# Kernel tuning notes

Hardware: AMD Instinct MI355X
Metric: run time of the kernel (lower is better)

## Reference

```python
import jax, jax.numpy as jnp
import numpy as np

B, S, H, V, L = 2, 1024, 2048, 32000, 8


def _ternary(w):
    """BitNet-1.58 style per-tensor ternary quantization with STE."""
    scale = jnp.mean(jnp.abs(w))
    wq = jnp.clip(jnp.round(w / (scale + 1e-8)), -1.0, 1.0) * scale
    # straight-through: forward value is wq, gradient flows to w
    return w + jax.lax.stop_gradient(wq - w)


def _layernorm(x, g, b, eps=1e-5):
    m = jnp.mean(x, axis=-1, keepdims=True)
    v = jnp.var(x, axis=-1, keepdims=True)
    return (x - m) / jnp.sqrt(v + eps) * g + b


def setup_inputs() -> dict:
    key = jax.random.key(0)
    ks = jax.random.split(key, 5)
    return {
        "input_ids": jax.random.randint(ks[0], (B, S), 0, V),
        "embed": jax.random.normal(ks[1], (V, H), jnp.float32) * 0.02,
        "layer_w": jax.random.normal(ks[2], (L, H, H), jnp.float32) * 0.02,
        "layer_b": jnp.zeros((L, H), jnp.float32),
        "ln_g": jnp.ones((L, H), jnp.float32),
        "ln_b": jnp.zeros((L, H), jnp.float32),
        "final_g": jnp.ones((H,), jnp.float32),
        "final_b": jnp.zeros((H,), jnp.float32),
        "head_w": jax.random.normal(ks[3], (V, H), jnp.float32) * 0.02,
    }


def reference(input_ids, embed, layer_w, layer_b, ln_g, ln_b, final_g, final_b, head_w):
    # embedding lookup: (B, S, H)
    h = embed[input_ids]

    def step(h, params):
        w, b, g, bb = params
        y = jnp.einsum("bsh,oh->bso", h, _ternary(w)) + b  # ternary linear
        h = _layernorm(y + h, g, bb)                        # residual + LN
        return h, None

    h, _ = jax.lax.scan(step, h, (layer_w, layer_b, ln_g, ln_b))
    h = _layernorm(h, final_g, final_b)
    logits = jnp.einsum("bsh,vh->bsv", h, _ternary(head_w))  # (B, S, V)
    return logits
```

## Files before the change

### kernel.cpp

```cpp
#include <hip/hip_runtime.h>


#define H 2048
#define MTOK 2048
#define VOC 32000
#define NL 8
#define BK 32

typedef __attribute__((ext_vector_type(8))) _Float16 f16x8;
typedef __attribute__((ext_vector_type(4))) float f32x4;

__device__ __forceinline__ unsigned short f2h(float f) {
  _Float16 h = (_Float16)f;
  union { _Float16 h; unsigned short u; } v; v.h = h;
  return v.u;
}

__global__ void abssum_kernel(const float* __restrict__ w, int n, float* __restrict__ out) {
  __shared__ float sbuf[4];
  int tid = blockIdx.x * blockDim.x + threadIdx.x;
  int stride = gridDim.x * blockDim.x * 4;
  float s = 0.f;
  for (int i = tid * 4; i < n; i += stride) {
    float4 v = *reinterpret_cast<const float4*>(w + i);
    s += fabsf(v.x) + fabsf(v.y) + fabsf(v.z) + fabsf(v.w);
  }
#pragma unroll
  for (int off = 32; off > 0; off >>= 1) s += __shfl_down(s, off);
  if ((threadIdx.x & 63) == 0) sbuf[threadIdx.x >> 6] = s;
  __syncthreads();
  if (threadIdx.x == 0) atomicAdd(out, sbuf[0] + sbuf[1] + sbuf[2] + sbuf[3]);
}

__global__ void quantize_kernel(const float* __restrict__ w, int n,
                                const float* __restrict__ sumptr, float cnt,
                                unsigned short* __restrict__ T) {
  float scale = *sumptr / cnt;
  float spe = scale + 1e-8f;
  int tid = blockIdx.x * blockDim.x + threadIdx.x;
  int stride = gridDim.x * blockDim.x * 4;
  for (int i = tid * 4; i < n; i += stride) {
    float4 v = *reinterpret_cast<const float4*>(w + i);
    ushort4 t;
    t.x = f2h(fminf(fmaxf(rintf(v.x / spe), -1.f), 1.f));
    t.y = f2h(fminf(fmaxf(rintf(v.y / spe), -1.f), 1.f));
    t.z = f2h(fminf(fmaxf(rintf(v.z / spe), -1.f), 1.f));
    t.w = f2h(fminf(fmaxf(rintf(v.w / spe), -1.f), 1.f));
    *reinterpret_cast<ushort4*>(T + i) = t;
  }
}

__global__ void gather_split_kernel(const int* __restrict__ ids, const float* __restrict__ embed,
                                    float* __restrict__ h, unsigned short* __restrict__ act) {
  int t = blockIdx.x;
  long src = (long)ids[t] * H;
  long dst = (long)t * H;
  for (int c = threadIdx.x * 4; c < H; c += blockDim.x * 4) {
    float4 v = *reinterpret_cast<const float4*>(embed + src + c);
    *reinterpret_cast<float4*>(h + dst + c) = v;
    ushort4 u;
    u.x = f2h(v.x); u.y = f2h(v.y); u.z = f2h(v.z); u.w = f2h(v.w);
    *reinterpret_cast<ushort4*>(act + dst + c) = u;
  }
}

__device__ __forceinline__ float block_sum(float v, float* sbuf) {
#pragma unroll
  for (int off = 32; off > 0; off >>= 1) v += __shfl_down(v, off);
  int lane = threadIdx.x & 63, w = threadIdx.x >> 6;
  if (lane == 0) sbuf[w] = v;
  __syncthreads();
  float r = sbuf[0] + sbuf[1] + sbuf[2] + sbuf[3];
  __syncthreads();
  return r;
}

__global__ void ln_kernel(const float* __restrict__ x_in, const float* __restrict__ resid,
                          const float* __restrict__ g, const float* __restrict__ b,
                          float* __restrict__ hout, unsigned short* __restrict__ act) {
  __shared__ float sbuf[4];
  int t = blockIdx.x;
  long base = (long)t * H;
  int c0 = threadIdx.x * 8;
  float x[8];
#pragma unroll
  for (int j = 0; j < 8; j += 4) {
    float4 v = *reinterpret_cast<const float4*>(x_in + base + c0 + j);
    x[j] = v.x; x[j + 1] = v.y; x[j + 2] = v.z; x[j + 3] = v.w;
  }
  if (resid != nullptr) {
#pragma unroll
    for (int j = 0; j < 8; j += 4) {
      float4 v = *reinterpret_cast<const float4*>(resid + base + c0 + j);
      x[j] += v.x; x[j + 1] += v.y; x[j + 2] += v.z; x[j + 3] += v.w;
    }
  }
  float s = 0.f;
#pragma unroll
  for (int j = 0; j < 8; ++j) s += x[j];
  s = block_sum(s, sbuf);
  float m = s * (1.f / H);
  float vs = 0.f;
#pragma unroll
  for (int j = 0; j < 8; ++j) { float d = x[j] - m; vs += d * d; }
  vs = block_sum(vs, sbuf);
  float r = 1.f / sqrtf(vs * (1.f / H) + 1e-5f);
  float o[8];
#pragma unroll
  for (int j = 0; j < 8; ++j) o[j] = (x[j] - m) * r * g[c0 + j] + b[c0 + j];
  if (hout != nullptr) {
#pragma unroll
    for (int j = 0; j < 8; j += 4) {
      float4 v; v.x = o[j]; v.y = o[j + 1]; v.z = o[j + 2]; v.w = o[j + 3];
      *reinterpret_cast<float4*>(hout + base + c0 + j) = v;
    }
  }
#pragma unroll
  for (int j = 0; j < 8; j += 4) {
    ushort4 u;
    u.x = f2h(o[j]); u.y = f2h(o[j + 1]); u.z = f2h(o[j + 2]); u.w = f2h(o[j + 3]);
    *reinterpret_cast<ushort4*>(act + base + c0 + j) = u;
  }
}

__device__ __forceinline__ void gll16(const void* g, void* l) {
  __builtin_amdgcn_global_load_lds((const __attribute__((address_space(1))) void*)g,
                                   (__attribute__((address_space(3))) void*)l, 16, 0, 0);
}

template <int ROWS>
__device__ __forceinline__ void stage_tile(unsigned short* sdst, const unsigned short* G,
                                           long row0, int k0, long ldk, int tid) {
#pragma unroll
  for (int i = 0; i < ROWS / 64; ++i) {
    int blk = i * 4 + (tid >> 6);
    int s = blk * 64 + (tid & 63);
    int row = s >> 2, col = (s & 3) * 8;
    const unsigned short* g = G + (row0 + row) * ldk + (k0 + col);
    gll16((const void*)g, (void*)(sdst + blk * 512));
  }
}

template <int TBM, int TBN, int WR, int WC, int MF, int NF, bool HAS_BIAS>
__global__ __launch_bounds__(256)
void gemm_t(const unsigned short* __restrict__ A, const unsigned short* __restrict__ Bt,
            const float* __restrict__ bias, const float* __restrict__ sumptr, float cnt,
            float* __restrict__ C, int N, int K, int nrb) {
  __shared__ unsigned short sA[TBM * BK];
  __shared__ unsigned short sB[TBN * BK];
  int tid = threadIdx.x;
  int lane = tid & 63, wid = tid >> 6;
  int wr = wid / WC, wc = wid % WC;

  int nwg = gridDim.x;
  int bid = blockIdx.x;
  int chunk = nwg >> 3;
  int swz = (bid & 7) * chunk + (bid >> 3);
  int rb = swz % nrb, cb = swz / nrb;
  long row0 = (long)rb * TBM;
  long col0 = (long)cb * TBN;

  f32x4 acc[MF][NF] = {};

  for (int k0 = 0; k0 < K; k0 += BK) {
    stage_tile<TBM>(sA, A, row0, k0, K, tid);
    stage_tile<TBN>(sB, Bt, col0, k0, K, tid);
    __syncthreads();

    f16x8 af[MF], bf[NF];
    int kb = (lane >> 4) * 8;
    int rsel = lane & 15;
#pragma unroll
    for (int f = 0; f < MF; ++f) {
      int ra = wr * (MF * 16) + f * 16 + rsel;
      af[f] = *reinterpret_cast<const f16x8*>(&sA[ra * BK + kb]);
    }
#pragma unroll
    for (int f = 0; f < NF; ++f) {
      int rbn = wc * (NF * 16) + f * 16 + rsel;
      bf[f] = *reinterpret_cast<const f16x8*>(&sB[rbn * BK + kb]);
    }
#pragma unroll
    for (int mf = 0; mf < MF; ++mf)
#pragma unroll
      for (int nf = 0; nf < NF; ++nf)
        acc[mf][nf] = __builtin_amdgcn_mfma_f32_16x16x32_f16(af[mf], bf[nf], acc[mf][nf], 0, 0, 0);
    __syncthreads();
  }

  float scale = *sumptr / cnt;
#pragma unroll
  for (int mf = 0; mf < MF; ++mf) {
    long grow0 = row0 + wr * (MF * 16) + mf * 16 + (lane >> 4) * 4;
#pragma unroll
    for (int nf = 0; nf < NF; ++nf) {
      long gcol = col0 + wc * (NF * 16) + nf * 16 + (lane & 15);
      float bv = HAS_BIAS ? bias[gcol] : 0.f;
#pragma unroll
      for (int r = 0; r < 4; ++r) {
        C[(grow0 + r) * (long)N + gcol] = acc[mf][nf][r] * scale + bv;
      }
    }
  }
}

extern "C" void kernel_launch(void* const* d_in, const int* in_sizes, int n_in,
                              void* d_out, int out_size, void* d_ws, size_t ws_size,
                              hipStream_t stream) {
  const int* input_ids = (const int*)d_in[0];
  const float* embed   = (const float*)d_in[1];
  const float* layer_w = (const float*)d_in[2];
  const float* layer_b = (const float*)d_in[3];
  const float* ln_g    = (const float*)d_in[4];
  const float* ln_b    = (const float*)d_in[5];
  const float* final_g = (const float*)d_in[6];
  const float* final_b = (const float*)d_in[7];
  const float* head_w  = (const float*)d_in[8];
  float* out = (float*)d_out;

  char* ws = (char*)d_ws;
  size_t off = 0;
  auto take = [&](size_t bytes) -> void* {
    void* p = ws + off;
    off = (off + bytes + 255) & ~(size_t)255;
    return p;
  };
  float* sums        = (float*)take(16 * sizeof(float));
  unsigned short* Tl = (unsigned short*)take((size_t)H * H * 2);
  unsigned short* Th = (unsigned short*)take((size_t)VOC * H * 2);
  float* hbuf        = (float*)take((size_t)MTOK * H * 4);
  float* ybuf        = (float*)take((size_t)MTOK * H * 4);
  unsigned short* act = (unsigned short*)take((size_t)MTOK * H * 2);
  (void)ws_size; (void)in_sizes; (void)n_in; (void)out_size;

  hipMemsetAsync(sums, 0, 16 * sizeof(float), stream);

  for (int l = 0; l < NL; ++l)
    abssum_kernel<<<512, 256, 0, stream>>>(layer_w + (size_t)l * H * H, H * H, sums + l);
  abssum_kernel<<<2048, 256, 0, stream>>>(head_w, VOC * H, sums + 8);

  quantize_kernel<<<4096, 256, 0, stream>>>(head_w, VOC * H, sums + 8, (float)((size_t)VOC * H), Th);

  gather_split_kernel<<<MTOK, 256, 0, stream>>>(input_ids, embed, hbuf, act);

  for (int l = 0; l < NL; ++l) {
    quantize_kernel<<<1024, 256, 0, stream>>>(layer_w + (size_t)l * H * H, H * H, sums + l,
                                              (float)(H * H), Tl);
    gemm_t<128, 64, 4, 1, 2, 4, true><<<512, 256, 0, stream>>>(
        act, Tl, layer_b + (size_t)l * H, sums + l, (float)(H * H), ybuf, H, H, MTOK / 128);
    ln_kernel<<<MTOK, 256, 0, stream>>>(ybuf, hbuf, ln_g + (size_t)l * H, ln_b + (size_t)l * H,
                                        hbuf, act);
  }

  ln_kernel<<<MTOK, 256, 0, stream>>>(hbuf, nullptr, final_g, final_b, nullptr, act);

  gemm_t<128, 128, 2, 2, 4, 4, false><<<4000, 256, 0, stream>>>(
      act, Th, nullptr, sums + 8, (float)((size_t)VOC * H), out, VOC, H, MTOK / 128);
}
```

Measured before the change: 1.581 ms.

## Double-buffer GEMM LDS tiles with BK=64, XOR swizzle, and batched abssum

The GEMM k-tile grows from 32 to 64 and uses two shared-memory buffers, so the next tile's global-to-LDS loads are issued while MFMAs run on the current one. One barrier per iteration replaces two. LDS placement uses an XOR swizzle of 16-byte segments to reduce bank conflicts on fragment reads. The eight per-layer abssum launches are merged into a single 2D-grid launch to cut launch overhead. LDS use doubles, which may lower occupancy.

```diff
diff --git a/kernel.cpp b/kernel.cpp
--- a/kernel.cpp
+++ b/kernel.cpp
@@ -5,7 +5,7 @@
 #define MTOK 2048
 #define VOC 32000
 #define NL 8
-#define BK 32
+#define BK 64
 
 typedef __attribute__((ext_vector_type(8))) _Float16 f16x8;
 typedef __attribute__((ext_vector_type(4))) float f32x4;
@@ -16,20 +16,22 @@
   return v.u;
 }
 
-__global__ void abssum_kernel(const float* __restrict__ w, int n, float* __restrict__ out) {
+__global__ void abssum_kernel(const float* __restrict__ w, int n, long nstride,
+                              float* __restrict__ out) {
   __shared__ float sbuf[4];
+  const float* wp = w + (long)blockIdx.y * nstride;
   int tid = blockIdx.x * blockDim.x + threadIdx.x;
   int stride = gridDim.x * blockDim.x * 4;
   float s = 0.f;
   for (int i = tid * 4; i < n; i += stride) {
-    float4 v = *reinterpret_cast<const float4*>(w + i);
+    float4 v = *reinterpret_cast<const float4*>(wp + i);
     s += fabsf(v.x) + fabsf(v.y) + fabsf(v.z) + fabsf(v.w);
   }
 #pragma unroll
   for (int off = 32; off > 0; off >>= 1) s += __shfl_down(s, off);
   if ((threadIdx.x & 63) == 0) sbuf[threadIdx.x >> 6] = s;
   __syncthreads();
-  if (threadIdx.x == 0) atomicAdd(out, sbuf[0] + sbuf[1] + sbuf[2] + sbuf[3]);
+  if (threadIdx.x == 0) atomicAdd(out + blockIdx.y, sbuf[0] + sbuf[1] + sbuf[2] + sbuf[3]);
 }
 
 __global__ void quantize_kernel(const float* __restrict__ w, int n,
@@ -131,12 +133,15 @@
 template <int ROWS>
 __device__ __forceinline__ void stage_tile(unsigned short* sdst, const unsigned short* G,
                                            long row0, int k0, long ldk, int tid) {
-#pragma unroll
-  for (int i = 0; i < ROWS / 64; ++i) {
-    int blk = i * 4 + (tid >> 6);
-    int s = blk * 64 + (tid & 63);
-    int row = s >> 2, col = (s & 3) * 8;
-    const unsigned short* g = G + (row0 + row) * ldk + (k0 + col);
+  int wv = tid >> 6, lane = tid & 63;
+  int c = lane & 7;
+  int r8 = lane >> 3;
+  int cs = c ^ r8;
+#pragma unroll
+  for (int i = 0; i < ROWS / 32; ++i) {
+    int blk = i * 4 + wv;
+    int row = blk * 8 + r8;
+    const unsigned short* g = G + (row0 + row) * ldk + (k0 + cs * 8);
     gll16((const void*)g, (void*)(sdst + blk * 512));
   }
 }
@@ -146,8 +151,8 @@
 void gemm_t(const unsigned short* __restrict__ A, const unsigned short* __restrict__ Bt,
             const float* __restrict__ bias, const float* __restrict__ sumptr, float cnt,
             float* __restrict__ C, int N, int K, int nrb) {
-  __shared__ unsigned short sA[TBM * BK];
-  __shared__ unsigned short sB[TBN * BK];
+  __shared__ unsigned short sA[2][TBM * BK];
+  __shared__ unsigned short sB[2][TBN * BK];
   int tid = threadIdx.x;
   int lane = tid & 63, wid = tid >> 6;
   int wr = wid / WC, wc = wid % WC;
@@ -156,45 +161,58 @@
   int bid = blockIdx.x;
   int chunk = nwg >> 3;
   int swz = (bid & 7) * chunk + (bid >> 3);
-  int rb = swz % nrb, cb = swz / nrb;
+  int rb = swz % nrb, cbl = swz / nrb;
   long row0 = (long)rb * TBM;
-  long col0 = (long)cb * TBN;
+  long col0 = (long)cbl * TBN;
 
   f32x4 acc[MF][NF] = {};
 
-  for (int k0 = 0; k0 < K; k0 += BK) {
-    stage_tile<TBM>(sA, A, row0, k0, K, tid);
-    stage_tile<TBN>(sB, Bt, col0, k0, K, tid);
+  int rsel = lane & 15;
+  int hi = lane >> 4;
+  int lx = lane & 7;
+
+  int NT = K >> 6;
+  stage_tile<TBM>(sA[0], A, row0, 0, K, tid);
+  stage_tile<TBN>(sB[0], Bt, col0, 0, K, tid);
+
+  for (int t = 0; t < NT; ++t) {
     __syncthreads();
-
-    f16x8 af[MF], bf[NF];
-    int kb = (lane >> 4) * 8;
-    int rsel = lane & 15;
-#pragma unroll
-    for (int f = 0; f < MF; ++f) {
-      int ra = wr * (MF * 16) + f * 16 + rsel;
-      af[f] = *reinterpret_cast<const f16x8*>(&sA[ra * BK + kb]);
-    }
-#pragma unroll
-    for (int f = 0; f < NF; ++f) {
-      int rbn = wc * (NF * 16) + f * 16 + rsel;
-      bf[f] = *reinterpret_cast<const f16x8*>(&sB[rbn * BK + kb]);
-    }
-#pragma unroll
-    for (int mf = 0; mf < MF; ++mf)
-#pragma unroll
-      for (int nf = 0; nf < NF; ++nf)
-        acc[mf][nf] = __builtin_amdgcn_mfma_f32_16x16x32_f16(af[mf], bf[nf], acc[mf][nf], 0, 0, 0);
-    __syncthreads();
+    int nb = (t + 1) & 1;
+    if (t + 1 < NT) {
+      stage_tile<TBM>(sA[nb], A, row0, (t + 1) << 6, K, tid);
+      stage_tile<TBN>(sB[nb], Bt, col0, (t + 1) << 6, K, tid);
+    }
+    const unsigned short* pA = sA[t & 1];
+    const unsigned short* pB = sB[t & 1];
+#pragma unroll
+    for (int kk = 0; kk < 2; ++kk) {
+      int seg = (kk * 4 + hi) ^ lx;
+      f16x8 af[MF], bf[NF];
+#pragma unroll
+      for (int f = 0; f < MF; ++f) {
+        int ra = wr * (MF * 16) + f * 16 + rsel;
+        af[f] = *reinterpret_cast<const f16x8*>(&pA[ra * BK + seg * 8]);
+      }
+#pragma unroll
+      for (int f = 0; f < NF; ++f) {
+        int rn = wc * (NF * 16) + f * 16 + rsel;
+        bf[f] = *reinterpret_cast<const f16x8*>(&pB[rn * BK + seg * 8]);
+      }
+#pragma unroll
+      for (int mf = 0; mf < MF; ++mf)
+#pragma unroll
+        for (int nf = 0; nf < NF; ++nf)
+          acc[mf][nf] = __builtin_amdgcn_mfma_f32_16x16x32_f16(af[mf], bf[nf], acc[mf][nf], 0, 0, 0);
+    }
   }
 
   float scale = *sumptr / cnt;
 #pragma unroll
   for (int mf = 0; mf < MF; ++mf) {
-    long grow0 = row0 + wr * (MF * 16) + mf * 16 + (lane >> 4) * 4;
+    long grow0 = row0 + wr * (MF * 16) + mf * 16 + hi * 4;
 #pragma unroll
     for (int nf = 0; nf < NF; ++nf) {
-      long gcol = col0 + wc * (NF * 16) + nf * 16 + (lane & 15);
+      long gcol = col0 + wc * (NF * 16) + nf * 16 + rsel;
       float bv = HAS_BIAS ? bias[gcol] : 0.f;
 #pragma unroll
       for (int r = 0; r < 4; ++r) {
@@ -235,9 +253,8 @@
 
   hipMemsetAsync(sums, 0, 16 * sizeof(float), stream);
 
-  for (int l = 0; l < NL; ++l)
-    abssum_kernel<<<512, 256, 0, stream>>>(layer_w + (size_t)l * H * H, H * H, sums + l);
-  abssum_kernel<<<2048, 256, 0, stream>>>(head_w, VOC * H, sums + 8);
+  abssum_kernel<<<dim3(512, NL), 256, 0, stream>>>(layer_w, H * H, (long)H * H, sums);
+  abssum_kernel<<<dim3(2048, 1), 256, 0, stream>>>(head_w, VOC * H, 0, sums + 8);
 
   quantize_kernel<<<4096, 256, 0, stream>>>(head_w, VOC * H, sums + 8, (float)((size_t)VOC * H), Th);
 
```

Result: faster. 1.478 ms (-6.5%).
